# Performance work log

Measured on AMD Instinct MI355X. Metric: run time of the kernel, lower is better.

## Reference

```python
import jax, jax.numpy as jnp
import numpy as np

D_MODEL = 512
HEADS = 8
WIN = 16
LN_EPS = 1e-5


def setup_inputs() -> dict:
    key = jax.random.key(0)
    ks = jax.random.split(key, 5)
    B, T = 2, 4096
    s = 1.0 / np.sqrt(D_MODEL)
    x = jax.random.normal(ks[0], (B, T, D_MODEL), dtype=jnp.float32)
    Wq = jax.random.normal(ks[1], (D_MODEL, D_MODEL), dtype=jnp.float32) * s
    Wk = jax.random.normal(ks[2], (D_MODEL, D_MODEL), dtype=jnp.float32) * s
    Wv = jax.random.normal(ks[3], (D_MODEL, D_MODEL), dtype=jnp.float32) * s
    Wp = jax.random.normal(ks[4], (D_MODEL, D_MODEL), dtype=jnp.float32) * s
    ln_gamma = jnp.ones((D_MODEL,), dtype=jnp.float32)
    ln_beta = jnp.zeros((D_MODEL,), dtype=jnp.float32)
    return {"x": x, "Wq": Wq, "Wk": Wk, "Wv": Wv, "Wp": Wp,
            "ln_gamma": ln_gamma, "ln_beta": ln_beta}


def _local_attention(x, Wq, Wk, Wv, Wp, ln_gamma, ln_beta):
    B, T, D = x.shape
    H = HEADS
    d = D // H
    scale = d ** (-0.5)
    # projections (torch Linear: y = x @ W^T)
    q = (x @ Wq.T).reshape(B, T, H, d)
    k = (x @ Wk.T).reshape(B, T, H, d)
    v = (x @ Wv.T).reshape(B, T, H, d)
    offs = jnp.arange(-WIN, WIN + 1)                      # [W]
    pos = jnp.arange(T)[:, None] + offs[None, :]          # [T, W]
    valid = (pos >= 0) & (pos < T)                        # [T, W]
    idx = jnp.clip(pos, 0, T - 1)                         # [T, W]
    k_win = k[:, idx]                                     # [B, T, W, H, d]
    v_win = v[:, idx]                                     # [B, T, W, H, d]
    scores = jnp.einsum('bthd,btwhd->bthw', q, k_win) * scale
    scores = jnp.where(valid[None, :, None, :], scores, -jnp.inf)
    attn = jax.nn.softmax(scores, axis=-1)                # over window
    out = jnp.einsum('bthw,btwhd->bthd', attn, v_win).reshape(B, T, D)
    y = x + out @ Wp.T                                    # residual + proj
    mu = jnp.mean(y, axis=-1, keepdims=True)
    var = jnp.mean(jnp.square(y - mu), axis=-1, keepdims=True)
    return ln_gamma * (y - mu) * jax.lax.rsqrt(var + LN_EPS) + ln_beta


def reference(x, Wq, Wk, Wv, Wp, ln_gamma, ln_beta):
    return _local_attention(x, Wq, Wk, Wv, Wp, ln_gamma, ln_beta)
```

## Files before the change

### kernel.cpp

```cpp
#include <hip/hip_runtime.h>
#include <hip/hip_bf16.h>
#include <stdint.h>

typedef __bf16 bf16;
typedef __attribute__((ext_vector_type(8))) __bf16 bf16x8;
typedef __attribute__((ext_vector_type(2))) __bf16 bf16x2;
typedef __attribute__((ext_vector_type(4))) float f32x4;
typedef __attribute__((ext_vector_type(4))) unsigned int u32x4;

#define GLOAD16(gsrc, ldst)                                              \
  __builtin_amdgcn_global_load_lds(                                      \
      (const __attribute__((address_space(1))) unsigned int*)(gsrc),     \
      (__attribute__((address_space(3))) unsigned int*)(ldst), 16, 0, 0)

static constexpr int T_LEN = 4096;
static constexpr int WIN = 16;

__device__ __forceinline__ bf16x8 cvt8(float4 a, float4 b) {
  bf16x8 o;
  o[0] = (bf16)a.x; o[1] = (bf16)a.y; o[2] = (bf16)a.z; o[3] = (bf16)a.w;
  o[4] = (bf16)b.x; o[5] = (bf16)b.y; o[6] = (bf16)b.z; o[7] = (bf16)b.w;
  return o;
}

__global__ __launch_bounds__(256) void prep_kernel(const float* __restrict__ x,
                                                   const float* __restrict__ wq,
                                                   const float* __restrict__ wk,
                                                   const float* __restrict__ wv,
                                                   const float* __restrict__ wp,
                                                   bf16* __restrict__ xb,
                                                   bf16* __restrict__ wqkv,
                                                   bf16* __restrict__ wpb) {
  int bid = blockIdx.x;
  if (bid < 2048) {
    int i = bid * 256 + threadIdx.x;
    const float4* s4 = (const float4*)x + (size_t)i * 2;
    ((bf16x8*)xb)[i] = cvt8(s4[0], s4[1]);
  } else {
    int i = (bid - 2048) * 256 + threadIdx.x;
    int which = i >> 15;
    int j = i & 32767;
    const float* src = (which == 0) ? wq : (which == 1) ? wk : (which == 2) ? wv : wp;
    bf16* dst = (which < 3) ? (wqkv + (size_t)which * 512 * 512) : wpb;
    const float4* s4 = (const float4*)src + (size_t)j * 2;
    ((bf16x8*)dst)[j] = cvt8(s4[0], s4[1]);
  }
}

__global__ __launch_bounds__(256) void gemm_qkv_kernel(const bf16* __restrict__ Ab,
                                                       const bf16* __restrict__ Bw,
                                                       bf16* __restrict__ Cb) {
  constexpr int K = 512, BK = 64, NIT = K / BK;
  __shared__ __align__(16) bf16 As[8192];
  __shared__ __align__(16) bf16 Bs[4096];
  const int tid = threadIdx.x;
  const int l = tid & 63;
  const int w = tid >> 6;
  const int g = l >> 4;
  const int c = l & 15;
  int bid = blockIdx.x;
  bid = (bid & 7) * 192 + (bid >> 3);
  const int m0 = (bid / 24) * 128;
  const int n0 = (bid % 24) * 64;

  const int wm = (w >> 1) * 64;
  const int wn = (w & 1) * 32;
  const int cx = c & 7;

  const f32x4 zero = {0.f, 0.f, 0.f, 0.f};
  f32x4 acc[4][2];
#pragma unroll
  for (int i = 0; i < 4; ++i)
#pragma unroll
    for (int j = 0; j < 2; ++j) acc[i][j] = zero;

#pragma unroll 1
  for (int t = 0; t < NIT; ++t) {
    const int k0 = t * BK;
#pragma unroll
    for (int i = 0; i < 4; ++i) {
      int s = tid + i * 256;
      int row = s >> 3;
      int j = s & 7;
      GLOAD16(Ab + (size_t)(m0 + row) * 512 + k0 + ((j ^ (row & 7)) << 3),
              &As[s * 8]);
    }
#pragma unroll
    for (int i = 0; i < 2; ++i) {
      int s = tid + i * 256;
      int row = s >> 3;
      int j = s & 7;
      GLOAD16(Bw + (size_t)(n0 + row) * 512 + k0 + ((j ^ (row & 7)) << 3),
              &Bs[s * 8]);
    }
    __syncthreads();
#pragma unroll
    for (int kk = 0; kk < 2; ++kk) {
      const int joff = ((kk * 4 + g) ^ cx) << 3;
      bf16x8 af[4], bfr[2];
#pragma unroll
      for (int mi = 0; mi < 4; ++mi)
        af[mi] = *(const bf16x8*)&As[(wm + mi * 16 + c) * 64 + joff];
#pragma unroll
      for (int ni = 0; ni < 2; ++ni)
        bfr[ni] = *(const bf16x8*)&Bs[(wn + ni * 16 + c) * 64 + joff];
#pragma unroll
      for (int mi = 0; mi < 4; ++mi)
#pragma unroll
        for (int ni = 0; ni < 2; ++ni)
          acc[mi][ni] = __builtin_amdgcn_mfma_f32_16x16x32_bf16(af[mi], bfr[ni], acc[mi][ni], 0, 0, 0);
    }
    __syncthreads();
  }

  bf16* Cw = &As[w * 2048];
  const int r0 = (l >> 4) * 4;
#pragma unroll
  for (int mi = 0; mi < 4; ++mi)
#pragma unroll
    for (int ni = 0; ni < 2; ++ni)
#pragma unroll
      for (int r = 0; r < 4; ++r)
        Cw[(mi * 16 + r0 + r) * 32 + ni * 16 + c] = (bf16)acc[mi][ni][r];
#pragma unroll
  for (int i = 0; i < 4; ++i) {
    int row = (l >> 2) + 16 * i;
    bf16x8 v = *(const bf16x8*)&Cw[row * 32 + (l & 3) * 8];
    *(bf16x8*)(Cb + (size_t)(m0 + wm + row) * 1536 + n0 + wn + (l & 3) * 8) = v;
  }
}

__global__ __launch_bounds__(512) void attn_proj_ln_kernel(
    const bf16* __restrict__ qkv, const bf16* __restrict__ Bw,
    const float* __restrict__ X, const float* __restrict__ gamma,
    const float* __restrict__ beta, float* __restrict__ out) {
  __shared__ __align__(16) bf16 POOL[63744];
  bf16* KV = POOL;
  bf16* Pp = POOL + 36864;
  bf16* aoutL = POOL + 46080;
  float* rsum = (float*)(POOL + 62720);
  float* rsq  = (float*)(POOL + 63232);

  const int tid = threadIdx.x;
  const int w = tid >> 6;
  const int l = tid & 63;
  const int g = l >> 4;
  const int c = l & 15;
  const int cx = c & 7;
  int bid = blockIdx.x;
  bid = (bid & 7) * 32 + (bid >> 3);
  const int m0 = bid * 32;
  const int b = m0 >> 12;
  const int tloc0 = m0 & (T_LEN - 1);
  const int base = b * T_LEN;

  const f32x4 zero = {0.f, 0.f, 0.f, 0.f};
  const u32x4 zu = {0u, 0u, 0u, 0u};
  const float scale = 0.125f;

  if (tid < 256) {
    int hl = tid >> 6;
    int row = tid & 63;
    *(uint4*)&KV[18432 + hl * 4608 + row * 72 + 64] = make_uint4(0u, 0u, 0u, 0u);
  }

#pragma unroll 1
  for (int pass = 0; pass < 2; ++pass) {
    if (pass) __syncthreads();
#pragma unroll
    for (int i = 0; i < 4; ++i) {
      int task = tid + i * 512;
      int hl = task >> 9;
      int rem = task & 511;
      int pp = rem >> 3;
      int c8 = (rem & 7) * 8;
      int h = pass * 4 + hl;
      int pg = base + min(max(tloc0 - WIN + pp, 0), T_LEN - 1);
      const bf16* kr = qkv + (size_t)pg * 1536 + 512 + h * 64 + c8;
      const bf16* vr = qkv + (size_t)pg * 1536 + 1024 + h * 64 + c8;
      *(bf16x8*)&KV[hl * 4608 + pp * 72 + c8] = *(const bf16x8*)kr;
      bf16x8 vv = *(const bf16x8*)vr;
      bf16* vt = &KV[18432 + hl * 4608];
#pragma unroll
      for (int e = 0; e < 8; ++e) vt[(c8 + e) * 72 + pp] = vv[e];
    }
    __syncthreads();

    const int hl = w >> 1;
    const int wh = w & 1;
    const int h = pass * 4 + hl;
    const int tg = tloc0 + wh * 16;
    bf16* Kl = &KV[hl * 4608];
    bf16* Vt = &KV[18432 + hl * 4608];

    const bf16* qrow = qkv + (size_t)(base + tg + c) * 1536 + h * 64;
    bf16x8 qf0 = *(const bf16x8*)(qrow + g * 8);
    bf16x8 qf1 = *(const bf16x8*)(qrow + 32 + g * 8);

    f32x4 st[3];
#pragma unroll
    for (int wt = 0; wt < 3; ++wt) {
      int rk = 16 * wh + 16 * wt + c;
      bf16x8 ka0 = *(const bf16x8*)&Kl[rk * 72 + g * 8];
      bf16x8 ka1 = *(const bf16x8*)&Kl[rk * 72 + 32 + g * 8];
      f32x4 t = __builtin_amdgcn_mfma_f32_16x16x32_bf16(ka0, qf0, zero, 0, 0, 0);
      st[wt] = __builtin_amdgcn_mfma_f32_16x16x32_bf16(ka1, qf1, t, 0, 0, 0);
    }

    float pv[3][4];
    float lsum = 0.f;
#pragma unroll
    for (int wt = 0; wt < 3; ++wt)
#pragma unroll
      for (int r = 0; r < 4; ++r) {
        int ww = 16 * wt + 4 * g + r;
        int pos = tg - WIN + ww;
        bool valid = (ww >= c) && (ww <= c + 32) && (pos >= 0) && (pos < T_LEN);
        float e = __expf(st[wt][r] * scale);
        pv[wt][r] = valid ? e : 0.f;
        lsum += pv[wt][r];
      }
    lsum += __shfl_xor(lsum, 16);
    lsum += __shfl_xor(lsum, 32);
    float inv = 1.f / lsum;

    bf16* P = &Pp[w * 1152];
#pragma unroll
    for (int wt = 0; wt < 3; ++wt) {
      bf16x2 p01, p23;
      p01[0] = (bf16)(pv[wt][0] * inv);
      p01[1] = (bf16)(pv[wt][1] * inv);
      p23[0] = (bf16)(pv[wt][2] * inv);
      p23[1] = (bf16)(pv[wt][3] * inv);
      *(bf16x2*)&P[c * 56 + 16 * wt + 4 * g]     = p01;
      *(bf16x2*)&P[c * 56 + 16 * wt + 4 * g + 2] = p23;
    }

    bf16x8 pa0 = *(const bf16x8*)&P[c * 56 + 8 * g];
    int g1 = (g < 2) ? g : 1;
    bf16x8 pa1 = *(const bf16x8*)&P[c * 56 + 32 + 8 * g1];
    if (g >= 2) pa1 = __builtin_bit_cast(bf16x8, zu);

    const int off0 = 16 * wh + 8 * g;
    const int off1 = 16 * wh + ((g < 2) ? 32 + 8 * g : 48);
    f32x4 acc[4] = {zero, zero, zero, zero};
#pragma unroll
    for (int dt = 0; dt < 4; ++dt) {
      bf16x8 v0 = *(const bf16x8*)&Vt[(16 * dt + c) * 72 + off0];
      bf16x8 v1 = *(const bf16x8*)&Vt[(16 * dt + c) * 72 + off1];
      acc[dt] = __builtin_amdgcn_mfma_f32_16x16x32_bf16(pa0, v0, acc[dt], 0, 0, 0);
      acc[dt] = __builtin_amdgcn_mfma_f32_16x16x32_bf16(pa1, v1, acc[dt], 0, 0, 0);
    }

#pragma unroll
    for (int dt = 0; dt < 4; ++dt)
#pragma unroll
      for (int r = 0; r < 4; ++r)
        aoutL[(wh * 16 + 4 * g + r) * 520 + h * 64 + 16 * dt + c] = (bf16)acc[dt][r];
  }

  bf16x8 breg[8];
#pragma unroll
  for (int i = 0; i < 8; ++i) {
    int s = tid + i * 512;
    int row = s >> 3;
    int j = s & 7;
    breg[i] = *(const bf16x8*)(Bw + (size_t)row * 512 + ((j ^ (row & 7)) << 3));
  }
  __syncthreads();

  f32x4 acc2[2][4];
#pragma unroll
  for (int m = 0; m < 2; ++m)
#pragma unroll
    for (int n = 0; n < 4; ++n) acc2[m][n] = zero;

#pragma unroll 1
  for (int t = 0; t < 8; ++t) {
    const int k0 = t * 64;
#pragma unroll
    for (int i = 0; i < 8; ++i) {
      int s = tid + i * 512;
      *(bf16x8*)&KV[s * 8] = breg[i];
    }
    __syncthreads();
    if (t < 7) {
      const int k1 = k0 + 64;
#pragma unroll
      for (int i = 0; i < 8; ++i) {
        int s = tid + i * 512;
        int row = s >> 3;
        int j = s & 7;
        breg[i] = *(const bf16x8*)(Bw + (size_t)row * 512 + k1 + ((j ^ (row & 7)) << 3));
      }
    }
#pragma unroll
    for (int kk = 0; kk < 2; ++kk) {
      const int joff = ((kk * 4 + g) ^ cx) << 3;
      bf16x8 af[2], bfv[4];
#pragma unroll
      for (int m = 0; m < 2; ++m)
        af[m] = *(const bf16x8*)&aoutL[(m * 16 + c) * 520 + k0 + (kk * 4 + g) * 8];
#pragma unroll
      for (int n = 0; n < 4; ++n)
        bfv[n] = *(const bf16x8*)&KV[(w * 64 + n * 16 + c) * 64 + joff];
#pragma unroll
      for (int m = 0; m < 2; ++m)
#pragma unroll
        for (int n = 0; n < 4; ++n)
          acc2[m][n] = __builtin_amdgcn_mfma_f32_16x16x32_bf16(af[m], bfv[n], acc2[m][n], 0, 0, 0);
    }
    __syncthreads();
  }

  const int col0 = w * 64 + c;
  float ps[2][4], ps2[2][4];
#pragma unroll
  for (int m = 0; m < 2; ++m)
#pragma unroll
    for (int r = 0; r < 4; ++r) {
      int row = m0 + m * 16 + 4 * g + r;
      float s = 0.f, s2 = 0.f;
#pragma unroll
      for (int n = 0; n < 4; ++n) {
        float y = acc2[m][n][r] + X[(size_t)row * 512 + col0 + n * 16];
        acc2[m][n][r] = y;
        s += y;
        s2 += y * y;
      }
      ps[m][r] = s;
      ps2[m][r] = s2;
    }
#pragma unroll
  for (int m = 0; m < 2; ++m)
#pragma unroll
    for (int r = 0; r < 4; ++r) {
      float s = ps[m][r], s2 = ps2[m][r];
      s += __shfl_xor(s, 1);  s2 += __shfl_xor(s2, 1);
      s += __shfl_xor(s, 2);  s2 += __shfl_xor(s2, 2);
      s += __shfl_xor(s, 4);  s2 += __shfl_xor(s2, 4);
      s += __shfl_xor(s, 8);  s2 += __shfl_xor(s2, 8);
      ps[m][r] = s;
      ps2[m][r] = s2;
    }
  if (c == 0) {
#pragma unroll
    for (int m = 0; m < 2; ++m)
#pragma unroll
      for (int r = 0; r < 4; ++r) {
        rsum[(m * 16 + 4 * g + r) * 8 + w] = ps[m][r];
        rsq[(m * 16 + 4 * g + r) * 8 + w] = ps2[m][r];
      }
  }
  __syncthreads();

  float gam[4], bet[4];
#pragma unroll
  for (int n = 0; n < 4; ++n) {
    gam[n] = gamma[col0 + n * 16];
    bet[n] = beta[col0 + n * 16];
  }
#pragma unroll
  for (int m = 0; m < 2; ++m)
#pragma unroll
    for (int r = 0; r < 4; ++r) {
      int rl = m * 16 + 4 * g + r;
      float sum = 0.f, sq = 0.f;
#pragma unroll
      for (int j = 0; j < 8; ++j) {
        sum += rsum[rl * 8 + j];
        sq += rsq[rl * 8 + j];
      }
      float mu = sum * (1.f / 512.f);
      float var = sq * (1.f / 512.f) - mu * mu;
      float rs = rsqrtf(var + 1e-5f);
#pragma unroll
      for (int n = 0; n < 4; ++n)
        out[(size_t)(m0 + rl) * 512 + col0 + n * 16] =
            gam[n] * (acc2[m][n][r] - mu) * rs + bet[n];
    }
}

extern "C" void kernel_launch(void* const* d_in, const int* in_sizes, int n_in,
                              void* d_out, int out_size, void* d_ws, size_t ws_size,
                              hipStream_t stream) {
  const float* x  = (const float*)d_in[0];
  const float* Wq = (const float*)d_in[1];
  const float* Wk = (const float*)d_in[2];
  const float* Wv = (const float*)d_in[3];
  const float* Wp = (const float*)d_in[4];
  const float* g  = (const float*)d_in[5];
  const float* be = (const float*)d_in[6];
  float* out = (float*)d_out;

  char* ws = (char*)d_ws;
  bf16* xb   = (bf16*)(ws);
  bf16* wqkv = (bf16*)(ws + 8388608);
  bf16* wpb  = (bf16*)(ws + 9961472);
  bf16* qkv  = (bf16*)(ws + 10485760);

  prep_kernel<<<2560, 256, 0, stream>>>(x, Wq, Wk, Wv, Wp, xb, wqkv, wpb);
  gemm_qkv_kernel<<<1536, 256, 0, stream>>>(xb, wqkv, qkv);
  attn_proj_ln_kernel<<<256, 512, 0, stream>>>(qkv, wpb, x, g, be, out);
}
```

Measured before the change: 54.82 us.

## Fuse fp32-to-bf16 conversion into GEMM and projection loads, drop prep kernel

Removes the separate prep kernel that converted x and all weights to bf16. The QKV GEMM now reads fp32 x and Wq/Wk/Wv directly, converts them in registers and stores bf16 to shared memory. The attention/projection kernel does the same for Wp. This saves one launch and the bf16 write-then-reread round trip. In exchange the async global_load_lds path is lost, and each GEMM block rereads fp32 data, which is twice the bytes of bf16, with the conversion redone across the 24 column tiles.

```diff
diff --git a/kernel.cpp b/kernel.cpp
--- a/kernel.cpp
+++ b/kernel.cpp
@@ -7,11 +7,6 @@
 typedef __attribute__((ext_vector_type(2))) __bf16 bf16x2;
 typedef __attribute__((ext_vector_type(4))) float f32x4;
 typedef __attribute__((ext_vector_type(4))) unsigned int u32x4;
-
-#define GLOAD16(gsrc, ldst)                                              \
-  __builtin_amdgcn_global_load_lds(                                      \
-      (const __attribute__((address_space(1))) unsigned int*)(gsrc),     \
-      (__attribute__((address_space(3))) unsigned int*)(ldst), 16, 0, 0)
 
 static constexpr int T_LEN = 4096;
 static constexpr int WIN = 16;
@@ -23,32 +18,10 @@
   return o;
 }
 
-__global__ __launch_bounds__(256) void prep_kernel(const float* __restrict__ x,
-                                                   const float* __restrict__ wq,
-                                                   const float* __restrict__ wk,
-                                                   const float* __restrict__ wv,
-                                                   const float* __restrict__ wp,
-                                                   bf16* __restrict__ xb,
-                                                   bf16* __restrict__ wqkv,
-                                                   bf16* __restrict__ wpb) {
-  int bid = blockIdx.x;
-  if (bid < 2048) {
-    int i = bid * 256 + threadIdx.x;
-    const float4* s4 = (const float4*)x + (size_t)i * 2;
-    ((bf16x8*)xb)[i] = cvt8(s4[0], s4[1]);
-  } else {
-    int i = (bid - 2048) * 256 + threadIdx.x;
-    int which = i >> 15;
-    int j = i & 32767;
-    const float* src = (which == 0) ? wq : (which == 1) ? wk : (which == 2) ? wv : wp;
-    bf16* dst = (which < 3) ? (wqkv + (size_t)which * 512 * 512) : wpb;
-    const float4* s4 = (const float4*)src + (size_t)j * 2;
-    ((bf16x8*)dst)[j] = cvt8(s4[0], s4[1]);
-  }
-}
-
-__global__ __launch_bounds__(256) void gemm_qkv_kernel(const bf16* __restrict__ Ab,
-                                                       const bf16* __restrict__ Bw,
+__global__ __launch_bounds__(256) void gemm_qkv_kernel(const float* __restrict__ Xf,
+                                                       const float* __restrict__ Wq,
+                                                       const float* __restrict__ Wk,
+                                                       const float* __restrict__ Wv,
                                                        bf16* __restrict__ Cb) {
   constexpr int K = 512, BK = 64, NIT = K / BK;
   __shared__ __align__(16) bf16 As[8192];
@@ -62,6 +35,8 @@
   bid = (bid & 7) * 192 + (bid >> 3);
   const int m0 = (bid / 24) * 128;
   const int n0 = (bid % 24) * 64;
+  const float* Bsrc = (n0 < 512) ? Wq : (n0 < 1024) ? Wk : Wv;
+  const int nr0 = n0 & 511;
 
   const int wm = (w >> 1) * 64;
   const int wn = (w & 1) * 32;
@@ -82,16 +57,20 @@
       int s = tid + i * 256;
       int row = s >> 3;
       int j = s & 7;
-      GLOAD16(Ab + (size_t)(m0 + row) * 512 + k0 + ((j ^ (row & 7)) << 3),
-              &As[s * 8]);
+      int ksrc = k0 + ((j ^ (row & 7)) << 3);
+      const float4* ap = (const float4*)(Xf + (size_t)(m0 + row) * 512 + ksrc);
+      float4 a0 = ap[0], a1 = ap[1];
+      *(bf16x8*)&As[s * 8] = cvt8(a0, a1);
     }
 #pragma unroll
     for (int i = 0; i < 2; ++i) {
       int s = tid + i * 256;
       int row = s >> 3;
       int j = s & 7;
-      GLOAD16(Bw + (size_t)(n0 + row) * 512 + k0 + ((j ^ (row & 7)) << 3),
-              &Bs[s * 8]);
+      int ksrc = k0 + ((j ^ (row & 7)) << 3);
+      const float4* bp = (const float4*)(Bsrc + (size_t)(nr0 + row) * 512 + ksrc);
+      float4 b0 = bp[0], b1 = bp[1];
+      *(bf16x8*)&Bs[s * 8] = cvt8(b0, b1);
     }
     __syncthreads();
 #pragma unroll
@@ -131,7 +110,7 @@
 }
 
 __global__ __launch_bounds__(512) void attn_proj_ln_kernel(
-    const bf16* __restrict__ qkv, const bf16* __restrict__ Bw,
+    const bf16* __restrict__ qkv, const float* __restrict__ Wp,
     const float* __restrict__ X, const float* __restrict__ gamma,
     const float* __restrict__ beta, float* __restrict__ out) {
   __shared__ __align__(16) bf16 POOL[63744];
@@ -182,7 +161,8 @@
       bf16x8 vv = *(const bf16x8*)vr;
       bf16* vt = &KV[18432 + hl * 4608];
 #pragma unroll
-      for (int e = 0; e < 8; ++e) vt[(c8 + e) * 72 + pp] = vv[e];
+      for (int e = 0; e < 8; ++e)
+        vt[(c8 + e) * 72 + pp] = vv[e];
     }
     __syncthreads();
 
@@ -265,7 +245,8 @@
     int s = tid + i * 512;
     int row = s >> 3;
     int j = s & 7;
-    breg[i] = *(const bf16x8*)(Bw + (size_t)row * 512 + ((j ^ (row & 7)) << 3));
+    const float4* bp = (const float4*)(Wp + (size_t)row * 512 + ((j ^ (row & 7)) << 3));
+    breg[i] = cvt8(bp[0], bp[1]);
   }
   __syncthreads();
 
@@ -291,7 +272,9 @@
         int s = tid + i * 512;
         int row = s >> 3;
         int j = s & 7;
-        breg[i] = *(const bf16x8*)(Bw + (size_t)row * 512 + k1 + ((j ^ (row & 7)) << 3));
+        const float4* bp =
+            (const float4*)(Wp + (size_t)row * 512 + k1 + ((j ^ (row & 7)) << 3));
+        breg[i] = cvt8(bp[0], bp[1]);
       }
     }
 #pragma unroll
@@ -393,13 +376,8 @@
   const float* be = (const float*)d_in[6];
   float* out = (float*)d_out;
 
-  char* ws = (char*)d_ws;
-  bf16* xb   = (bf16*)(ws);
-  bf16* wqkv = (bf16*)(ws + 8388608);
-  bf16* wpb  = (bf16*)(ws + 9961472);
-  bf16* qkv  = (bf16*)(ws + 10485760);
-
-  prep_kernel<<<2560, 256, 0, stream>>>(x, Wq, Wk, Wv, Wp, xb, wqkv, wpb);
-  gemm_qkv_kernel<<<1536, 256, 0, stream>>>(xb, wqkv, qkv);
-  attn_proj_ln_kernel<<<256, 512, 0, stream>>>(qkv, wpb, x, g, be, out);
+  bf16* qkv = (bf16*)d_ws;
+
+  gemm_qkv_kernel<<<1536, 256, 0, stream>>>(x, Wq, Wk, Wv, qkv);
+  attn_proj_ln_kernel<<<256, 512, 0, stream>>>(qkv, Wp, x, g, be, out);
 }
```

Result: slower. 77.87 us (+42.0%).
